# Kernel tuning notes

Hardware: AMD Instinct MI355X
Metric: run time of the kernel (lower is better)

Reference implementation:

```python
import jax, jax.numpy as jnp
import numpy as np

EDGE_DROPOUT = 0.1   # init kwarg edge_dropout
TRAINING = True      # init kwarg is_training
N_NODES = 8192
D_FEAT = 512


def setup_inputs() -> dict:
    key = jax.random.key(0)
    x = jax.random.normal(key, (N_NODES, D_FEAT), dtype=jnp.float32)
    return {"x": x, "k": 30}


def _graph_process(x, k):
    # knn_fast: cosine similarity kNN with symmetric degree normalization.
    n = x.shape[0]
    xn = x / jnp.linalg.norm(x, axis=1, keepdims=True)      # F.normalize(x, dim=1)
    sim = xn @ xn.T                                         # [n, n] (torch does this in blocks of 1000; same math)
    vals, inds = jax.lax.top_k(sim, k + 1)                  # [n, k+1]
    rows = jnp.broadcast_to(jnp.arange(n)[:, None], vals.shape).reshape(-1)
    cols = inds.reshape(-1)
    v = vals.reshape(-1)
    norm_row = vals.sum(axis=1)                             # out-degree mass
    norm_col = jnp.zeros(n, vals.dtype).at[cols].add(v)     # in-degree mass (index_add_)
    norm = norm_row + norm_col
    v = v * (norm[rows] ** -0.5) * (norm[cols] ** -0.5)
    # values[torch.isnan(values)] = 0
    v = jnp.where(jnp.isnan(v), jnp.zeros_like(v), v)
    # symmetrize edge list
    rows_ = jnp.concatenate([rows, cols])
    cols_ = jnp.concatenate([cols, rows])
    v_ = jnp.concatenate([v, v])
    v_ = jax.nn.relu(v_)
    if TRAINING and EDGE_DROPOUT > 0.0:
        keep = jax.random.bernoulli(jax.random.key(42), 1.0 - EDGE_DROPOUT, v_.shape)
        v_ = jnp.where(keep, v_ / (1.0 - EDGE_DROPOUT), jnp.zeros_like(v_))
    # sparse_coo_tensor(...).coalesce(): duplicate (i,j) entries sum -> dense scatter-add
    adj = jnp.zeros((n, n), v_.dtype).at[rows_, cols_].add(v_)
    return adj


def reference(x, k):
    return _graph_process(x, k)
```

## Files before the change

### kernel.cpp

```cpp
#include <hip/hip_runtime.h>
#include <cstdint>
#include <cmath>

#define NN 8192
#define DD 512
#define KP1 31
#define HALF_EDGES (NN * KP1)

typedef float f2 __attribute__((ext_vector_type(2)));

__device__ __forceinline__ uint32_t rotl32(uint32_t v, int s) {
  return (v << s) | (v >> (32 - s));
}

__device__ __forceinline__ void threefry2x32_42(uint32_t x0, uint32_t x1,
                                                uint32_t& o0, uint32_t& o1) {
  const uint32_t ks0 = 0u, ks1 = 42u;
  const uint32_t ks2 = 0x1BD11BDAu ^ ks0 ^ ks1;
  x0 += ks0; x1 += ks1;
  x0 += x1; x1 = rotl32(x1, 13); x1 ^= x0;
  x0 += x1; x1 = rotl32(x1, 15); x1 ^= x0;
  x0 += x1; x1 = rotl32(x1, 26); x1 ^= x0;
  x0 += x1; x1 = rotl32(x1, 6);  x1 ^= x0;
  x0 += ks1; x1 += ks2 + 1u;
  x0 += x1; x1 = rotl32(x1, 17); x1 ^= x0;
  x0 += x1; x1 = rotl32(x1, 29); x1 ^= x0;
  x0 += x1; x1 = rotl32(x1, 16); x1 ^= x0;
  x0 += x1; x1 = rotl32(x1, 24); x1 ^= x0;
  x0 += ks2; x1 += ks0 + 2u;
  x0 += x1; x1 = rotl32(x1, 13); x1 ^= x0;
  x0 += x1; x1 = rotl32(x1, 15); x1 ^= x0;
  x0 += x1; x1 = rotl32(x1, 26); x1 ^= x0;
  x0 += x1; x1 = rotl32(x1, 6);  x1 ^= x0;
  x0 += ks0; x1 += ks1 + 3u;
  x0 += x1; x1 = rotl32(x1, 17); x1 ^= x0;
  x0 += x1; x1 = rotl32(x1, 29); x1 ^= x0;
  x0 += x1; x1 = rotl32(x1, 16); x1 ^= x0;
  x0 += x1; x1 = rotl32(x1, 24); x1 ^= x0;
  x0 += ks1; x1 += ks2 + 4u;
  x0 += x1; x1 = rotl32(x1, 13); x1 ^= x0;
  x0 += x1; x1 = rotl32(x1, 15); x1 ^= x0;
  x0 += x1; x1 = rotl32(x1, 26); x1 ^= x0;
  x0 += x1; x1 = rotl32(x1, 6);  x1 ^= x0;
  x0 += ks2; x1 += ks0 + 5u;
  o0 = x0; o1 = x1;
}

__device__ __forceinline__ bool keep_edge(uint32_t e) {
  uint32_t y0, y1;
  threefry2x32_42(0u, e, y0, y1);
  uint32_t bits = y0 ^ y1;
  float u = __uint_as_float((bits >> 9) | 0x3f800000u) - 1.0f;
  return u < 0.9f;
}

__device__ __forceinline__ void gll16(const float4* gsrc, void* lds) {
  __builtin_amdgcn_global_load_lds(
      (const __attribute__((address_space(1))) uint32_t*)gsrc,
      (__attribute__((address_space(3))) uint32_t*)lds, 16, 0, 0);
}

__global__ __launch_bounds__(256) void rownorm_kernel(const float* __restrict__ x,
                                                      float* __restrict__ nrm) {
#pragma clang fp contract(off)
  __shared__ float rowbuf[16][DD];
  __shared__ float partial[16][4];
  int tid = threadIdx.x;
  int rowbase = blockIdx.x * 16;

  for (int p = 0; p < 8; ++p) {
    int f = tid + p * 256;
    int r = f >> 7, k4 = f & 127;
    *(float4*)(&rowbuf[r][k4 << 2]) =
        *(const float4*)(x + (size_t)(rowbase + r) * DD + (k4 << 2));
  }
  __syncthreads();
  if (tid < 64) {
    int r = tid >> 2, q = tid & 3;
    const float* s = &rowbuf[r][q * 128];
    float a0 = s[0]*s[0], a1 = s[1]*s[1], a2 = s[2]*s[2], a3 = s[3]*s[3];
    float a4 = s[4]*s[4], a5 = s[5]*s[5], a6 = s[6]*s[6], a7 = s[7]*s[7];
    for (int i = 8; i < 128; i += 8) {
      a0 += s[i+0]*s[i+0]; a1 += s[i+1]*s[i+1];
      a2 += s[i+2]*s[i+2]; a3 += s[i+3]*s[i+3];
      a4 += s[i+4]*s[i+4]; a5 += s[i+5]*s[i+5];
      a6 += s[i+6]*s[i+6]; a7 += s[i+7]*s[i+7];
    }
    partial[r][q] = ((a0 + a1) + (a2 + a3)) + ((a4 + a5) + (a6 + a7));
  }
  __syncthreads();
  if (tid < 16) {
    float S = (partial[tid][0] + partial[tid][1]) + (partial[tid][2] + partial[tid][3]);
    nrm[rowbase + tid] = sqrtf(S);
  }
}

__global__ __launch_bounds__(256) void xnorm_kernel(const float* __restrict__ x,
                                                    const float* __restrict__ nrm,
                                                    float* __restrict__ xn) {
#pragma clang fp contract(off)
  int idx = blockIdx.x * 256 + threadIdx.x;
  const float4* xv = (const float4*)x;
  float4* xo = (float4*)xn;
  float4 v = xv[idx];
  float n = nrm[idx >> 7];
  v.x = v.x / n; v.y = v.y / n; v.z = v.z / n; v.w = v.w / n;
  xo[idx] = v;
}

__global__ __launch_bounds__(256, 2) void gemm_kernel_pre(const float* __restrict__ x,
                                                          float* __restrict__ out) {
#pragma clang fp contract(off)
  int bid = blockIdx.x;
  int by = (int)((129.0f - sqrtf(16641.0f - 8.0f * (float)bid)) * 0.5f);
  while (64 * by - (by * (by - 1)) / 2 > bid) --by;
  while (64 * (by + 1) - ((by + 1) * by) / 2 <= bid) ++by;
  const int bx = by + (bid - (64 * by - (by * (by - 1)) / 2));

  __shared__ __align__(16) char smem[32768];
  float4* AsF4 = (float4*)smem;
  float*  Bs   = (float*)(smem + 16384);

  const int tid = threadIdx.x;
  const int rb = by * 128;
  const int cb = bx * 128;
  const int m = tid & 3;
  const int g = tid >> 2;

  const int lane = tid & 63, wave = tid >> 6;
  const int wr = wave >> 1, wc = wave & 1;
  const int lr = lane >> 3, lc = lane & 7;
  const int r0 = wr * 64 + lr * 8;
  const int c0 = wc * 64 + lc * 8;
  const int r3 = r0 >> 3;

  f2 acc[8][4];
  #pragma unroll
  for (int i = 0; i < 8; ++i)
    #pragma unroll
    for (int jp = 0; jp < 4; ++jp) { acc[i][jp].x = 0.f; acc[i][jp].y = 0.f; }

  const float4* xv = (const float4*)x;
  float4 rbv[2];

  int gr[2], gs[2];
  #pragma unroll
  for (int q = 0; q < 2; ++q) {
    int fi = wave * 128 + q * 64 + lane;
    gr[q] = fi >> 2;
    gs[q] = ((fi & 3) - (gr[q] >> 3)) & 3;
  }

  auto stage_A = [&](int nbuf, int t) {
    #pragma unroll
    for (int q = 0; q < 2; ++q)
      gll16(xv + (size_t)(rb + gr[q]) * 128 + t * 4 + gs[q],
            (void*)(AsF4 + nbuf * 512 + wave * 128 + q * 64));
  };
  auto load_B = [&](int t) {
    #pragma unroll
    for (int p = 0; p < 2; ++p)
      rbv[p] = xv[(size_t)(cb + g + 64 * p) * 128 + t * 4 + m];
  };
  auto write_B = [&](int nbuf) {
    #pragma unroll
    for (int p = 0; p < 2; ++p) {
      int r = g + 64 * p;
      float* bp = Bs + nbuf * 2048 + (4 * m) * 128 + (r ^ (m << 3));
      bp[0]   = rbv[p].x;
      bp[128] = rbv[p].y;
      bp[256] = rbv[p].z;
      bp[384] = rbv[p].w;
    }
  };

  load_B(0);
  write_B(0);
  stage_A(0, 0);
  load_B(1);

  #pragma unroll 1
  for (int t = 0; t < 32; ++t) {
    const int buf = t & 1;
    __syncthreads();
    if (t < 31) {
      stage_A(buf ^ 1, t + 1);
      write_B(buf ^ 1);
      if (t < 30) load_B(t + 2);
    }
    const float4* Ab = AsF4 + buf * 512;
    const float*  Bb = Bs + buf * 2048;
    #pragma unroll
    for (int k4 = 0; k4 < 4; ++k4) {
      float4 av[8];
      const int tA = (k4 + r3) & 3;
      #pragma unroll
      for (int i = 0; i < 8; ++i) av[i] = Ab[(r0 + i) * 4 + tA];
      const int csw = c0 ^ (k4 << 3);
      #pragma unroll
      for (int kk = 0; kk < 4; ++kk) {
        const float* bp = Bb + (4 * k4 + kk) * 128 + csw;
        float4 b0 = *(const float4*)(bp);
        float4 b1 = *(const float4*)(bp + 4);
        f2 bb0 = {b0.x, b0.y};
        f2 bb1 = {b0.z, b0.w};
        f2 bb2 = {b1.x, b1.y};
        f2 bb3 = {b1.z, b1.w};
        #pragma unroll
        for (int i = 0; i < 8; ++i) {
          float a = ((const float*)&av[i])[kk];
          f2 t0 = a * bb0;
          f2 t1 = a * bb1;
          f2 t2 = a * bb2;
          f2 t3 = a * bb3;
          acc[i][0] = acc[i][0] + t0;
          acc[i][1] = acc[i][1] + t1;
          acc[i][2] = acc[i][2] + t2;
          acc[i][3] = acc[i][3] + t3;
        }
      }
    }
  }

  float4* outv = (float4*)out;

  #pragma unroll
  for (int i = 0; i < 8; ++i) {
    #pragma unroll
    for (int h = 0; h < 2; ++h) {
      float4 o;
      o.x = acc[i][2 * h].x;     o.y = acc[i][2 * h].y;
      o.z = acc[i][2 * h + 1].x; o.w = acc[i][2 * h + 1].y;
      outv[(size_t)(rb + r0 + i) * 2048 + ((cb + c0) >> 2) + h] = o;
    }
  }

  if (rb != cb) {
    float* Cs = (float*)smem;
    #pragma unroll 1
    for (int q = 0; q < 4; ++q) {
      __syncthreads();
      if (wr == (q >> 1) && (lr >> 2) == (q & 1)) {
        const int rB = (lr & 3) * 8;
        #pragma unroll
        for (int i = 0; i < 8; ++i) {
          #pragma unroll
          for (int jp = 0; jp < 4; ++jp)
            *(f2*)(Cs + (rB + i) * 130 + wc * 64 + lc * 8 + 2 * jp) = acc[i][jp];
        }
      }
      __syncthreads();
      #pragma unroll
      for (int q2 = 0; q2 < 4; ++q2) {
        int f = tid + q2 * 256;
        int c = f >> 3, t4 = f & 7;
        float4 o;
        o.x = Cs[(4 * t4 + 0) * 130 + c];
        o.y = Cs[(4 * t4 + 1) * 130 + c];
        o.z = Cs[(4 * t4 + 2) * 130 + c];
        o.w = Cs[(4 * t4 + 3) * 130 + c];
        outv[(size_t)(cb + c) * 2048 + ((rb + q * 32) >> 2) + t4] = o;
      }
    }
  }
}

__global__ __launch_bounds__(256, 2) void gemm_kernel_fb(const float* __restrict__ x,
                                                         const float* __restrict__ nrm,
                                                         float* __restrict__ out) {
#pragma clang fp contract(off)
  int bid = blockIdx.x;
  int by = (int)((129.0f - sqrtf(16641.0f - 8.0f * (float)bid)) * 0.5f);
  while (64 * by - (by * (by - 1)) / 2 > bid) --by;
  while (64 * (by + 1) - ((by + 1) * by) / 2 <= bid) ++by;
  const int bx = by + (bid - (64 * by - (by * (by - 1)) / 2));

  extern __shared__ char smem[];
  float4* AsF4 = (float4*)smem;
  float*  Bs   = (float*)(smem + 16384);

  const int tid = threadIdx.x;
  const int rb = by * 128;
  const int cb = bx * 128;
  const int m = tid & 7;
  const int g = tid >> 3;

  float nA[4], nB[4];
  #pragma unroll
  for (int p = 0; p < 4; ++p) {
    nA[p] = nrm[rb + g + 32 * p];
    nB[p] = nrm[cb + g + 32 * p];
  }

  const int lane = tid & 63, wave = tid >> 6;
  const int wr = wave >> 1, wc = wave & 1;
  const int lr = lane >> 3, lc = lane & 7;
  const int r0 = wr * 64 + lr * 8;
  const int c0 = wc * 64 + lc * 8;
  const int r3 = r0 >> 3;

  f2 acc[8][4];
  #pragma unroll
  for (int i = 0; i < 8; ++i)
    #pragma unroll
    for (int jp = 0; jp < 4; ++jp) { acc[i][jp].x = 0.f; acc[i][jp].y = 0.f; }

  const float4* xv = (const float4*)x;
  float4 ra[4], rbv[4];
  #pragma unroll
  for (int p = 0; p < 4; ++p) {
    int r = g + 32 * p;
    ra[p]  = xv[(size_t)(rb + r) * 128 + m];
    rbv[p] = xv[(size_t)(cb + r) * 128 + m];
  }

  for (int kc = 0; kc < 16; ++kc) {
    __syncthreads();
    #pragma unroll
    for (int p = 0; p < 4; ++p) {
      int r = g + 32 * p;
      float4 va = ra[p];
      va.x = va.x / nA[p]; va.y = va.y / nA[p];
      va.z = va.z / nA[p]; va.w = va.w / nA[p];
      AsF4[r * 8 + ((m + (r >> 3)) & 7)] = va;
      float4 vb = rbv[p];
      vb.x = vb.x / nB[p]; vb.y = vb.y / nB[p];
      vb.z = vb.z / nB[p]; vb.w = vb.w / nB[p];
      float* bp = Bs + (4 * m) * 128 + (r ^ (m << 3));
      bp[0]   = vb.x;
      bp[128] = vb.y;
      bp[256] = vb.z;
      bp[384] = vb.w;
    }
    __syncthreads();
    if (kc < 15) {
      #pragma unroll
      for (int p = 0; p < 4; ++p) {
        int r = g + 32 * p;
        ra[p]  = xv[(size_t)(rb + r) * 128 + (kc + 1) * 8 + m];
        rbv[p] = xv[(size_t)(cb + r) * 128 + (kc + 1) * 8 + m];
      }
    }

    #pragma unroll 2
    for (int k4 = 0; k4 < 8; ++k4) {
      float4 av[8];
      const int tA = (k4 + r3) & 7;
      #pragma unroll
      for (int i = 0; i < 8; ++i) av[i] = AsF4[(r0 + i) * 8 + tA];
      float4 b01[8];
      const int csw = c0 ^ (k4 << 3);
      #pragma unroll
      for (int kk = 0; kk < 4; ++kk) {
        const float* bp = Bs + (4 * k4 + kk) * 128 + csw;
        b01[2 * kk]     = *(const float4*)(bp);
        b01[2 * kk + 1] = *(const float4*)(bp + 4);
      }
      #pragma unroll
      for (int kk = 0; kk < 4; ++kk) {
        f2 bb0 = {b01[2 * kk].x,     b01[2 * kk].y};
        f2 bb1 = {b01[2 * kk].z,     b01[2 * kk].w};
        f2 bb2 = {b01[2 * kk + 1].x, b01[2 * kk + 1].y};
        f2 bb3 = {b01[2 * kk + 1].z, b01[2 * kk + 1].w};
        #pragma unroll
        for (int i = 0; i < 8; ++i) {
          float a = ((const float*)&av[i])[kk];
          f2 t0 = a * bb0;
          f2 t1 = a * bb1;
          f2 t2 = a * bb2;
          f2 t3 = a * bb3;
          acc[i][0] = acc[i][0] + t0;
          acc[i][1] = acc[i][1] + t1;
          acc[i][2] = acc[i][2] + t2;
          acc[i][3] = acc[i][3] + t3;
        }
      }
    }
  }

  float4* outv = (float4*)out;
  #pragma unroll
  for (int i = 0; i < 8; ++i) {
    #pragma unroll
    for (int h = 0; h < 2; ++h) {
      float4 o;
      o.x = acc[i][2 * h].x;     o.y = acc[i][2 * h].y;
      o.z = acc[i][2 * h + 1].x; o.w = acc[i][2 * h + 1].y;
      outv[(size_t)(rb + r0 + i) * 2048 + ((cb + c0) >> 2) + h] = o;
    }
  }
  if (rb != cb) {
    float* Cs = (float*)smem;
    #pragma unroll 1
    for (int q = 0; q < 4; ++q) {
      __syncthreads();
      if (wr == (q >> 1) && (lr >> 2) == (q & 1)) {
        const int rB = (lr & 3) * 8;
        #pragma unroll
        for (int i = 0; i < 8; ++i) {
          #pragma unroll
          for (int jp = 0; jp < 4; ++jp)
            *(f2*)(Cs + (rB + i) * 130 + wc * 64 + lc * 8 + 2 * jp) = acc[i][jp];
        }
      }
      __syncthreads();
      #pragma unroll
      for (int q2 = 0; q2 < 4; ++q2) {
        int f = tid + q2 * 256;
        int c = f >> 3, t4 = f & 7;
        float4 o;
        o.x = Cs[(4 * t4 + 0) * 130 + c];
        o.y = Cs[(4 * t4 + 1) * 130 + c];
        o.z = Cs[(4 * t4 + 2) * 130 + c];
        o.w = Cs[(4 * t4 + 3) * 130 + c];
        outv[(size_t)(cb + c) * 2048 + ((rb + q * 32) >> 2) + t4] = o;
      }
    }
  }
}

__global__ __launch_bounds__(256) void topk_kernel(const float* __restrict__ sim,
                                                   float* __restrict__ vals,
                                                   int* __restrict__ inds) {
  const int w = threadIdx.x >> 6;
  const int lane = threadIdx.x & 63;
  const int row = blockIdx.x * 4 + w;

  float kval = -1e30f;
  int   kidx = 0;
  float kmin = -1e30f;

  const float* srow = sim + (size_t)row * NN;
  for (int grp = 0; grp < NN / 64; ++grp) {
    float v = srow[grp * 64 + lane];
    unsigned long long mask = __ballot(v > kmin);
    while (mask) {
      int src = __builtin_ctzll(mask);
      mask &= mask - 1;
      float vv = __shfl(v, src, 64);
      if (vv > kmin) {
        int cc = grp * 64 + src;
        unsigned long long ge = __ballot(kval >= vv) & 0x7FFFFFFFull;
        int pos = __popcll(ge);
        float upv = __shfl_up(kval, 1, 64);
        int   upi = __shfl_up(kidx, 1, 64);
        if (lane < KP1) {
          if (lane == pos) { kval = vv; kidx = cc; }
          else if (lane > pos) { kval = upv; kidx = upi; }
        }
        kmin = __shfl(kval, KP1 - 1, 64);
      }
    }
  }
  if (lane < KP1) {
    vals[(size_t)row * KP1 + lane] = kval;
    inds[row * KP1 + lane] = kidx;
  }
}

__global__ __launch_bounds__(256) void norm_kernel(const float* __restrict__ vals,
                                                   const int* __restrict__ inds,
                                                   float* __restrict__ norm) {
  int i = blockIdx.x * blockDim.x + threadIdx.x;
  if (i >= NN) return;
  float s = 0.f;
  for (int t = 0; t < KP1; ++t) {
    float v = vals[i * KP1 + t];
    s += v;
    atomicAdd(&norm[inds[i * KP1 + t]], v);
  }
  atomicAdd(&norm[i], s);
}

__global__ __launch_bounds__(256) void scatter_kernel(const float* __restrict__ vals,
                                                      const int* __restrict__ inds,
                                                      const float* __restrict__ norm,
                                                      float* __restrict__ out) {
  int e = blockIdx.x * blockDim.x + threadIdx.x;
  if (e >= HALF_EDGES) return;
  int i = e / KP1;
  int c = inds[e];
  float v = vals[e];
  float nv = v * (1.0f / sqrtf(norm[i])) * (1.0f / sqrtf(norm[c]));
  if (isnan(nv)) nv = 0.f;
  nv = fmaxf(nv, 0.f);
  float scaled = nv / 0.9f;
  if (keep_edge((uint32_t)e))
    atomicAdd(out + (size_t)i * NN + c, scaled);
  if (keep_edge((uint32_t)(e + HALF_EDGES)))
    atomicAdd(out + (size_t)c * NN + i, scaled);
}

extern "C" void kernel_launch(void* const* d_in, const int* in_sizes, int n_in,
                              void* d_out, int out_size, void* d_ws, size_t ws_size,
                              hipStream_t stream) {
  (void)in_sizes; (void)n_in;
  const float* x = (const float*)d_in[0];
  float* out = (float*)d_out;

  float* nrm  = (float*)d_ws;
  float* vals = nrm + NN;
  int*   inds = (int*)(vals + HALF_EDGES);
  float* norm = (float*)(inds + HALF_EDGES);
  float* xn   = (float*)((char*)d_ws + (size_t)(2 * 1024 * 1024));
  const bool pre = ws_size >= (size_t)(2 * 1024 * 1024) + (size_t)NN * DD * 4;

  hipLaunchKernelGGL(rownorm_kernel, dim3(NN / 16), dim3(256), 0, stream, x, nrm);
  if (pre) {
    hipLaunchKernelGGL(xnorm_kernel, dim3(NN * DD / 4 / 256), dim3(256), 0, stream,
                       x, nrm, xn);
    hipLaunchKernelGGL(gemm_kernel_pre, dim3(2080), dim3(256), 0, stream,
                       xn, out);
  } else {
    hipLaunchKernelGGL(gemm_kernel_fb, dim3(2080), dim3(256), 32768, stream,
                       x, nrm, out);
  }
  hipLaunchKernelGGL(topk_kernel, dim3(NN / 4), dim3(256), 0, stream,
                     out, vals, inds);
  hipMemsetAsync(norm, 0, NN * sizeof(float), stream);
  hipLaunchKernelGGL(norm_kernel, dim3((NN + 255) / 256), dim3(256), 0, stream,
                     vals, inds, norm);
  hipMemsetAsync(d_out, 0, (size_t)out_size * sizeof(float), stream);
  hipLaunchKernelGGL(scatter_kernel, dim3((HALF_EDGES + 255) / 256), dim3(256), 0, stream,
                     vals, inds, norm, out);
}
```

Baseline: 1.111 ms.

## Shrink GEMM K-tile, swizzle block order, vectorize topk scan, fuse norm into topk

```diff
diff --git a/kernel.cpp b/kernel.cpp
--- a/kernel.cpp
+++ b/kernel.cpp
@@ -111,21 +111,22 @@
 __global__ __launch_bounds__(256, 2) void gemm_kernel_pre(const float* __restrict__ x,
                                                           float* __restrict__ out) {
 #pragma clang fp contract(off)
-  int bid = blockIdx.x;
+  int bid0 = blockIdx.x;
+  int bid = (bid0 & 7) * 260 + (bid0 >> 3);
   int by = (int)((129.0f - sqrtf(16641.0f - 8.0f * (float)bid)) * 0.5f);
   while (64 * by - (by * (by - 1)) / 2 > bid) --by;
   while (64 * (by + 1) - ((by + 1) * by) / 2 <= bid) ++by;
   const int bx = by + (bid - (64 * by - (by * (by - 1)) / 2));
 
-  __shared__ __align__(16) char smem[32768];
+  __shared__ __align__(16) char smem[16384];
   float4* AsF4 = (float4*)smem;
-  float*  Bs   = (float*)(smem + 16384);
+  float*  Bs   = (float*)(smem + 8192);
 
   const int tid = threadIdx.x;
   const int rb = by * 128;
   const int cb = bx * 128;
-  const int m = tid & 3;
-  const int g = tid >> 2;
+  const int m = tid & 1;
+  const int g = tid >> 1;
 
   const int lane = tid & 63, wave = tid >> 6;
   const int wr = wave >> 1, wc = wave & 1;
@@ -141,37 +142,24 @@
     for (int jp = 0; jp < 4; ++jp) { acc[i][jp].x = 0.f; acc[i][jp].y = 0.f; }
 
   const float4* xv = (const float4*)x;
-  float4 rbv[2];
-
-  int gr[2], gs[2];
-  #pragma unroll
-  for (int q = 0; q < 2; ++q) {
-    int fi = wave * 128 + q * 64 + lane;
-    gr[q] = fi >> 2;
-    gs[q] = ((fi & 3) - (gr[q] >> 3)) & 3;
-  }
+  float4 rbv;
+
+  const int gr = tid >> 1;
+  const int gs = ((tid & 1) - (gr >> 3)) & 1;
 
   auto stage_A = [&](int nbuf, int t) {
-    #pragma unroll
-    for (int q = 0; q < 2; ++q)
-      gll16(xv + (size_t)(rb + gr[q]) * 128 + t * 4 + gs[q],
-            (void*)(AsF4 + nbuf * 512 + wave * 128 + q * 64));
+    gll16(xv + (size_t)(rb + gr) * 128 + t * 2 + gs,
+          (void*)(AsF4 + nbuf * 256 + wave * 64));
   };
   auto load_B = [&](int t) {
-    #pragma unroll
-    for (int p = 0; p < 2; ++p)
-      rbv[p] = xv[(size_t)(cb + g + 64 * p) * 128 + t * 4 + m];
+    rbv = xv[(size_t)(cb + g) * 128 + t * 2 + m];
   };
   auto write_B = [&](int nbuf) {
-    #pragma unroll
-    for (int p = 0; p < 2; ++p) {
-      int r = g + 64 * p;
-      float* bp = Bs + nbuf * 2048 + (4 * m) * 128 + (r ^ (m << 3));
-      bp[0]   = rbv[p].x;
-      bp[128] = rbv[p].y;
-      bp[256] = rbv[p].z;
-      bp[384] = rbv[p].w;
-    }
+    float* bp = Bs + nbuf * 1024 + (4 * m) * 128 + (g ^ (m << 3));
+    bp[0]   = rbv.x;
+    bp[128] = rbv.y;
+    bp[256] = rbv.z;
+    bp[384] = rbv.w;
   };
 
   load_B(0);
@@ -180,22 +168,22 @@
   load_B(1);
 
   #pragma unroll 1
-  for (int t = 0; t < 32; ++t) {
+  for (int t = 0; t < 64; ++t) {
     const int buf = t & 1;
     __syncthreads();
-    if (t < 31) {
+    if (t < 63) {
       stage_A(buf ^ 1, t + 1);
       write_B(buf ^ 1);
-      if (t < 30) load_B(t + 2);
-    }
-    const float4* Ab = AsF4 + buf * 512;
-    const float*  Bb = Bs + buf * 2048;
-    #pragma unroll
-    for (int k4 = 0; k4 < 4; ++k4) {
+      if (t < 62) load_B(t + 2);
+    }
+    const float4* Ab = AsF4 + buf * 256;
+    const float*  Bb = Bs + buf * 1024;
+    #pragma unroll
+    for (int k4 = 0; k4 < 2; ++k4) {
       float4 av[8];
-      const int tA = (k4 + r3) & 3;
-      #pragma unroll
-      for (int i = 0; i < 8; ++i) av[i] = Ab[(r0 + i) * 4 + tA];
+      const int tA = (k4 + r3) & 1;
+      #pragma unroll
+      for (int i = 0; i < 8; ++i) av[i] = Ab[(r0 + i) * 2 + tA];
       const int csw = c0 ^ (k4 << 3);
       #pragma unroll
       for (int kk = 0; kk < 4; ++kk) {
@@ -236,30 +224,22 @@
   }
 
   if (rb != cb) {
-    float* Cs = (float*)smem;
-    #pragma unroll 1
-    for (int q = 0; q < 4; ++q) {
-      __syncthreads();
-      if (wr == (q >> 1) && (lr >> 2) == (q & 1)) {
-        const int rB = (lr & 3) * 8;
-        #pragma unroll
-        for (int i = 0; i < 8; ++i) {
-          #pragma unroll
-          for (int jp = 0; jp < 4; ++jp)
-            *(f2*)(Cs + (rB + i) * 130 + wc * 64 + lc * 8 + 2 * jp) = acc[i][jp];
+    const int rq = (rb + r0) >> 2;
+    #pragma unroll
+    for (int jp = 0; jp < 4; ++jp) {
+      #pragma unroll
+      for (int h = 0; h < 2; ++h) {
+        const int col = c0 + 2 * jp + h;
+        float4 lo, hi;
+        if (h == 0) {
+          lo.x = acc[0][jp].x; lo.y = acc[1][jp].x; lo.z = acc[2][jp].x; lo.w = acc[3][jp].x;
+          hi.x = acc[4][jp].x; hi.y = acc[5][jp].x; hi.z = acc[6][jp].x; hi.w = acc[7][jp].x;
+        } else {
+          lo.x = acc[0][jp].y; lo.y = acc[1][jp].y; lo.z = acc[2][jp].y; lo.w = acc[3][jp].y;
+          hi.x = acc[4][jp].y; hi.y = acc[5][jp].y; hi.z = acc[6][jp].y; hi.w = acc[7][jp].y;
         }
-      }
-      __syncthreads();
-      #pragma unroll
-      for (int q2 = 0; q2 < 4; ++q2) {
-        int f = tid + q2 * 256;
-        int c = f >> 3, t4 = f & 7;
-        float4 o;
-        o.x = Cs[(4 * t4 + 0) * 130 + c];
-        o.y = Cs[(4 * t4 + 1) * 130 + c];
-        o.z = Cs[(4 * t4 + 2) * 130 + c];
-        o.w = Cs[(4 * t4 + 3) * 130 + c];
-        outv[(size_t)(cb + c) * 2048 + ((rb + q * 32) >> 2) + t4] = o;
+        outv[(size_t)(cb + col) * 2048 + rq]     = lo;
+        outv[(size_t)(cb + col) * 2048 + rq + 1] = hi;
       }
     }
   }
@@ -421,7 +401,8 @@
 
 __global__ __launch_bounds__(256) void topk_kernel(const float* __restrict__ sim,
                                                    float* __restrict__ vals,
-                                                   int* __restrict__ inds) {
+                                                   int* __restrict__ inds,
+                                                   float* __restrict__ norm) {
   const int w = threadIdx.x >> 6;
   const int lane = threadIdx.x & 63;
   const int row = blockIdx.x * 4 + w;
@@ -430,16 +411,28 @@
   int   kidx = 0;
   float kmin = -1e30f;
 
-  const float* srow = sim + (size_t)row * NN;
-  for (int grp = 0; grp < NN / 64; ++grp) {
-    float v = srow[grp * 64 + lane];
-    unsigned long long mask = __ballot(v > kmin);
-    while (mask) {
-      int src = __builtin_ctzll(mask);
-      mask &= mask - 1;
-      float vv = __shfl(v, src, 64);
+  const float4* srow = (const float4*)(sim + (size_t)row * NN);
+  for (int grp = 0; grp < NN / 256; ++grp) {
+    float4 v = srow[grp * 64 + lane];
+    unsigned long long m0 = __ballot(v.x > kmin);
+    unsigned long long m1 = __ballot(v.y > kmin);
+    unsigned long long m2 = __ballot(v.z > kmin);
+    unsigned long long m3 = __ballot(v.w > kmin);
+    while (m0 | m1 | m2 | m3) {
+      int c0_ = m0 ? 4 * __builtin_ctzll(m0) + 0 : 1024;
+      int c1_ = m1 ? 4 * __builtin_ctzll(m1) + 1 : 1024;
+      int c2_ = m2 ? 4 * __builtin_ctzll(m2) + 2 : 1024;
+      int c3_ = m3 ? 4 * __builtin_ctzll(m3) + 3 : 1024;
+      int cmin = min(min(c0_, c1_), min(c2_, c3_));
+      int e = cmin & 3, src = cmin >> 2;
+      if      (e == 0) m0 &= m0 - 1;
+      else if (e == 1) m1 &= m1 - 1;
+      else if (e == 2) m2 &= m2 - 1;
+      else             m3 &= m3 - 1;
+      float vsel = (e == 0) ? v.x : (e == 1) ? v.y : (e == 2) ? v.z : v.w;
+      float vv = __shfl(vsel, src, 64);
       if (vv > kmin) {
-        int cc = grp * 64 + src;
+        int cc = grp * 256 + cmin;
         unsigned long long ge = __ballot(kval >= vv) & 0x7FFFFFFFull;
         int pos = __popcll(ge);
         float upv = __shfl_up(kval, 1, 64);
@@ -456,20 +449,12 @@
     vals[(size_t)row * KP1 + lane] = kval;
     inds[row * KP1 + lane] = kidx;
   }
-}
-
-__global__ __launch_bounds__(256) void norm_kernel(const float* __restrict__ vals,
-                                                   const int* __restrict__ inds,
-                                                   float* __restrict__ norm) {
-  int i = blockIdx.x * blockDim.x + threadIdx.x;
-  if (i >= NN) return;
-  float s = 0.f;
-  for (int t = 0; t < KP1; ++t) {
-    float v = vals[i * KP1 + t];
-    s += v;
-    atomicAdd(&norm[inds[i * KP1 + t]], v);
-  }
-  atomicAdd(&norm[i], s);
+  float contrib = (lane < KP1) ? kval : 0.0f;
+  #pragma unroll
+  for (int off = 32; off; off >>= 1)
+    contrib += __shfl_xor(contrib, off, 64);
+  if (lane == 0) atomicAdd(&norm[row], contrib);
+  if (lane < KP1) atomicAdd(&norm[kidx], kval);
 }
 
 __global__ __launch_bounds__(256) void scatter_kernel(const float* __restrict__ vals,
@@ -506,6 +491,7 @@
   const bool pre = ws_size >= (size_t)(2 * 1024 * 1024) + (size_t)NN * DD * 4;
 
   hipLaunchKernelGGL(rownorm_kernel, dim3(NN / 16), dim3(256), 0, stream, x, nrm);
+  hipMemsetAsync(norm, 0, NN * sizeof(float), stream);
   if (pre) {
     hipLaunchKernelGGL(xnorm_kernel, dim3(NN * DD / 4 / 256), dim3(256), 0, stream,
                        x, nrm, xn);
@@ -516,10 +502,7 @@
                        x, nrm, out);
   }
   hipLaunchKernelGGL(topk_kernel, dim3(NN / 4), dim3(256), 0, stream,
-                     out, vals, inds);
-  hipMemsetAsync(norm, 0, NN * sizeof(float), stream);
-  hipLaunchKernelGGL(norm_kernel, dim3((NN + 255) / 256), dim3(256), 0, stream,
-                     vals, inds, norm);
+                     out, vals, inds, norm);
   hipMemsetAsync(d_out, 0, (size_t)out_size * sizeof(float), stream);
   hipLaunchKernelGGL(scatter_kernel, dim3((HALF_EDGES + 255) / 256), dim3(256), 0, stream,
                      vals, inds, norm, out);
```

Measured after the change: 1.286 ms. +15.7%, slower.
